# Performance work log

Hardware: AMD Instinct MI355X
Metric: run time of the kernel (lower is better)

The kernel has to match this reference:

```python
import jax, jax.numpy as jnp
import numpy as np

N = 16000
E = 128000
IN_DIM = 512
H1 = 4096
H2 = 1024
OUT_DIM = 64


def setup_inputs() -> dict:
    key = jax.random.key(0)
    ks = jax.random.split(key, 8)
    x = jax.random.normal(ks[0], (N, IN_DIM), dtype=jnp.float32)
    edge_index = jax.random.randint(ks[1], (2, E), 0, N, dtype=jnp.int64)

    def glorot(k, fan_in, fan_out):
        lim = float(np.sqrt(6.0 / (fan_in + fan_out)))
        return jax.random.uniform(k, (fan_in, fan_out), jnp.float32, -lim, lim)

    # PyG SAGEConv: out = lin_l(mean_j x_j) + lin_r(x); lin_l has bias, lin_r does not.
    params = {
        'W1l': glorot(ks[2], IN_DIM, H1), 'b1': jnp.zeros((H1,), jnp.float32),
        'W1r': glorot(ks[3], IN_DIM, H1),
        'W2l': glorot(ks[4], H1, H2), 'b2': jnp.zeros((H2,), jnp.float32),
        'W2r': glorot(ks[5], H1, H2),
        'W3l': glorot(ks[6], H2, OUT_DIM), 'b3': jnp.zeros((OUT_DIM,), jnp.float32),
        'W3r': glorot(ks[7], H2, OUT_DIM),
    }
    return {'x': x, 'edge_index': edge_index, **params}


def _sage_conv(x, src, dst, Wl, b, Wr):
    # mean-aggregate neighbor features at dst, then linear; plus root transform
    agg = jax.ops.segment_sum(x[src], dst, num_segments=N)          # [N, F_in]
    cnt = jax.ops.segment_sum(jnp.ones((src.shape[0],), x.dtype), dst, num_segments=N)
    mean = agg / jnp.maximum(cnt, 1.0)[:, None]
    return mean @ Wl + b + x @ Wr


def reference(x, edge_index, W1l, b1, W1r, W2l, b2, W2r, W3l, b3, W3r):
    src, dst = edge_index[0], edge_index[1]
    h = jax.nn.relu(_sage_conv(x, src, dst, W1l, b1, W1r))   # dropout is identity in eval
    h = jax.nn.relu(_sage_conv(h, src, dst, W2l, b2, W2r))
    h = _sage_conv(h, src, dst, W3l, b3, W3r)
    return jax.nn.log_softmax(h, axis=1)
```

## Files before the change

kernel.cpp:

```cpp
#include <hip/hip_runtime.h>
#include <stdint.h>

typedef __bf16 bf16x8 __attribute__((ext_vector_type(8)));
typedef float  f32x4  __attribute__((ext_vector_type(4)));
typedef const void __attribute__((address_space(1))) gv_t;
typedef void __attribute__((address_space(3))) sv_t;

static __device__ __forceinline__ unsigned short f2bf(float f) {
  unsigned u = __float_as_uint(f);
  u += 0x7fffu + ((u >> 16) & 1u);
  return (unsigned short)(u >> 16);
}
static __device__ __forceinline__ float bf2f(unsigned short h) {
  return __uint_as_float(((unsigned)h) << 16);
}
static __device__ __forceinline__ void gload16(const void* g, void* l) {
  __builtin_amdgcn_global_load_lds((gv_t*)g, (sv_t*)l, 16, 0, 0);
}

__global__ void k_sentinel(float* out, int n, float val) {
  int t = blockIdx.x * 256 + threadIdx.x;
  if (t < n) out[t] = val;
}
__global__ void k_zero(int* p, int n) {
  int t = blockIdx.x * 256 + threadIdx.x;
  if (t < n) p[t] = 0;
}

__global__ void k_detect(const int* ei, int* flag) {
  if (blockIdx.x == 0 && threadIdx.x == 0) {
    int nz = 0;
    for (int t = 0; t < 256; ++t) nz += (ei[2 * t + 1] != 0);
    *flag = (nz == 0) ? 1 : 0;
  }
}

__global__ void k_degree(const int* ei, int E, const int* flag, int* deg) {
  int t = blockIdx.x * 256 + threadIdx.x;
  if (t < E) {
    int d = (*flag) ? ei[2 * (E + t)] : ei[E + t];
    atomicAdd(&deg[d], 1);
  }
}
__global__ void k_scan(const int* deg, int* rp, int* cur, int n) {
  __shared__ int ssum[256];
  int t = threadIdx.x;
  int chunk = (n + 255) >> 8;
  int lo = t * chunk, hi = min(lo + chunk, n);
  int s = 0;
  for (int i = lo; i < hi; ++i) s += deg[i];
  ssum[t] = s;
  __syncthreads();
  if (t == 0) {
    int run = 0;
    for (int i = 0; i < 256; ++i) { int v = ssum[i]; ssum[i] = run; run += v; }
  }
  __syncthreads();
  int run = ssum[t];
  for (int i = lo; i < hi; ++i) { rp[i] = run; cur[i] = run; run += deg[i]; }
  if (t == 255) rp[n] = run;
}
__global__ void k_fill(const int* ei, int E, const int* flag, int* cur, int* col) {
  int t = blockIdx.x * 256 + threadIdx.x;
  if (t < E) {
    int f = *flag;
    int s = f ? ei[2 * t] : ei[t];
    int d = f ? ei[2 * (E + t)] : ei[E + t];
    int p = atomicAdd(&cur[d], 1);
    col[p] = s;
  }
}

__global__ void k_cvtx(const float4* __restrict__ in, ushort4* __restrict__ xm, int total4) {
  int t = blockIdx.x * 256 + threadIdx.x;
  if (t < total4) {
    int row = t >> 7, c = t & 127;
    float4 v = in[t];
    xm[(size_t)row * 256 + c] = make_ushort4(f2bf(v.x), f2bf(v.y), f2bf(v.z), f2bf(v.w));
  }
}

__global__ void k_transW(const float* W, unsigned short* Wt, int K, int N, int ld, int kofs) {
  __shared__ float tile[32][33];
  int tx = threadIdx.x & 31, ty = threadIdx.x >> 5;
  int n0 = blockIdx.x << 5, k0 = blockIdx.y << 5;
#pragma unroll
  for (int r = 0; r < 4; ++r)
    tile[ty + r * 8][tx] = W[(size_t)(k0 + ty + r * 8) * N + n0 + tx];
  __syncthreads();
#pragma unroll
  for (int r = 0; r < 4; ++r)
    Wt[(size_t)(n0 + ty + r * 8) * ld + kofs + k0 + tx] = f2bf(tile[tx][ty + r * 8]);
}

__global__ void k_agg(ushort4* __restrict__ xm, const int* __restrict__ rp,
                      const int* __restrict__ col) {
  int i = blockIdx.x;
  int s = rp[i], e = rp[i + 1];
  float inv = 1.0f / (float)max(e - s, 1);
  int f = threadIdx.x;
  float4 a = make_float4(0.f, 0.f, 0.f, 0.f);
  for (int n = s; n < e; ++n) {
    ushort4 v = xm[(size_t)col[n] * 256 + f];
    a.x += bf2f(v.x); a.y += bf2f(v.y); a.z += bf2f(v.z); a.w += bf2f(v.w);
  }
  xm[(size_t)i * 256 + 128 + f] =
      make_ushort4(f2bf(a.x * inv), f2bf(a.y * inv), f2bf(a.z * inv), f2bf(a.w * inv));
}

template <bool RELU, bool BIAS>
__global__ __launch_bounds__(512, 1) void k_gemm256(
    const unsigned short* __restrict__ A, const unsigned short* __restrict__ B,
    const float* __restrict__ bias, unsigned short* __restrict__ outp,
    int Mreal, int N, int K, int bnShift) {
  __shared__ __align__(16) unsigned short lds[2][2][256 * 64];

  const int tid = threadIdx.x;
  const int lane = tid & 63;
  const int wq = tid >> 6;
  const int wr = wq >> 2;
  const int wc = wq & 3;

  const int nwg = gridDim.x;
  const int q8 = nwg >> 3, r8 = nwg & 7;
  const int xcd = blockIdx.x & 7, idx = blockIdx.x >> 3;
  const int wg = (xcd < r8 ? xcd * (q8 + 1) : r8 * (q8 + 1) + (xcd - r8) * q8) + idx;
  const int bn = wg & ((1 << bnShift) - 1);
  const int bm = wg >> bnShift;

  const unsigned short* Ap = A + (size_t)bm * 256 * K;
  const unsigned short* Bp = B + (size_t)bn * 256 * K;
  const int sl8 = ((lane & 7) ^ (lane >> 3)) * 8;
  const int rsub = wq * 8 + (lane >> 3);

#define STAGE_A(BUF, I, K0)                                            \
  gload16(Ap + (size_t)((I) * 64 + rsub) * K + (K0) + sl8,             \
          (char*)&lds[BUF][0][0] + ((I) * 64 + wq * 8) * 128)
#define STAGE_B(BUF, I, K0)                                            \
  gload16(Bp + (size_t)((I) * 64 + rsub) * K + (K0) + sl8,             \
          (char*)&lds[BUF][1][0] + ((I) * 64 + wq * 8) * 128)
#define VMCNT(NUM) asm volatile("s_waitcnt vmcnt(" #NUM ")" ::: "memory")

  f32x4 acc[8][4];
#pragma unroll
  for (int m = 0; m < 8; ++m)
#pragma unroll
    for (int n = 0; n < 4; ++n) acc[m][n] = (f32x4){0.f, 0.f, 0.f, 0.f};

#define LOAD_AFR(DST, CUR, QA)                                                          \
  do {                                                                                  \
    const char* baseA = (const char*)&lds[CUR][0][0];                                   \
    _Pragma("unroll") for (int mm = 0; mm < 4; ++mm) {                                  \
      const int rr = ((QA) * 4 + mm) * 32 + wr * 16 + (lane & 15);                      \
      _Pragma("unroll") for (int kk = 0; kk < 2; ++kk)                                  \
          DST[mm][kk] = *(const bf16x8*)(baseA + rr * 128 +                             \
                                         (((kk * 4 + (lane >> 4)) ^ (lane & 7)) << 4)); \
    }                                                                                   \
  } while (0)
#define LOAD_BFR(DST, CUR, QB)                                                          \
  do {                                                                                  \
    const char* baseB = (const char*)&lds[CUR][1][0];                                   \
    _Pragma("unroll") for (int nn = 0; nn < 2; ++nn) {                                  \
      const int cc = ((QB) * 2 + nn) * 64 + wc * 16 + (lane & 15);                      \
      _Pragma("unroll") for (int kk = 0; kk < 2; ++kk)                                  \
          DST[nn][kk] = *(const bf16x8*)(baseB + cc * 128 +                             \
                                         (((kk * 4 + (lane >> 4)) ^ (lane & 7)) << 4)); \
    }                                                                                   \
  } while (0)
#define MFMA_Q(QA, QB, AFR, BFR)                                                        \
  do {                                                                                  \
    _Pragma("unroll") for (int mm = 0; mm < 4; ++mm)                                    \
        _Pragma("unroll") for (int nn = 0; nn < 2; ++nn)                                \
            _Pragma("unroll") for (int kk = 0; kk < 2; ++kk)                            \
                acc[(QA) * 4 + mm][(QB) * 2 + nn] =                                     \
                    __builtin_amdgcn_mfma_f32_16x16x32_bf16(                            \
                        AFR[mm][kk], BFR[nn][kk], acc[(QA) * 4 + mm][(QB) * 2 + nn],    \
                        0, 0, 0);                                                       \
  } while (0)

  STAGE_A(0, 0, 0); STAGE_A(0, 1, 0);
  STAGE_B(0, 0, 0); STAGE_B(0, 1, 0);
  STAGE_B(0, 2, 0); STAGE_B(0, 3, 0);
  STAGE_A(0, 2, 0); STAGE_A(0, 3, 0);
  STAGE_A(1, 0, 64); STAGE_A(1, 1, 64);
  STAGE_B(1, 0, 64); STAGE_B(1, 1, 64);
  STAGE_B(1, 2, 64); STAGE_B(1, 3, 64);
  STAGE_A(1, 2, 64); STAGE_A(1, 3, 64);
  VMCNT(8);
  __builtin_amdgcn_s_barrier();

  bf16x8 a0[4][2], b0[2][2], a1[4][2], b1[2][2];
  LOAD_AFR(a0, 0, 0);
  LOAD_BFR(b0, 0, 0);

  const int nt = K >> 6;
#pragma unroll 1
  for (int t = 0; t < nt; ++t) {
    const int cur = t & 1, nxt = cur ^ 1;
    const int k2 = (t + 2) << 6;
    LOAD_AFR(a1, cur, 1);
    LOAD_BFR(b1, cur, 1);
    __builtin_amdgcn_s_setprio(1);
    MFMA_Q(0, 0, a0, b0);
    __builtin_amdgcn_s_setprio(0);
    asm volatile("s_waitcnt lgkmcnt(0)" ::: "memory");
    __builtin_amdgcn_s_barrier();
    if (t + 2 < nt) {
      STAGE_A(cur, 0, k2); STAGE_A(cur, 1, k2);
      STAGE_B(cur, 0, k2); STAGE_B(cur, 1, k2);
      STAGE_B(cur, 2, k2); STAGE_B(cur, 3, k2);
      STAGE_A(cur, 2, k2); STAGE_A(cur, 3, k2);
    }
    __builtin_amdgcn_s_setprio(1);
    MFMA_Q(1, 0, a1, b0);
    MFMA_Q(0, 1, a0, b1);
    __builtin_amdgcn_s_setprio(0);
    if (t + 1 < nt) {
      if (t + 2 < nt) { VMCNT(8); } else { VMCNT(0); }
      __builtin_amdgcn_s_barrier();
      LOAD_AFR(a0, nxt, 0);
      LOAD_BFR(b0, nxt, 0);
    }
    __builtin_amdgcn_s_setprio(1);
    MFMA_Q(1, 1, a1, b1);
    __builtin_amdgcn_s_setprio(0);
  }

  const int row0 = bm * 256 + wr * 16 + ((lane >> 4) << 2);
  const int col0 = bn * 256 + wc * 16 + (lane & 15);
#pragma unroll
  for (int m = 0; m < 8; ++m) {
#pragma unroll
    for (int n = 0; n < 4; ++n) {
      const int col = col0 + n * 64;
      float bb = BIAS ? bias[col] : 0.f;
#pragma unroll
      for (int r = 0; r < 4; ++r) {
        int row = row0 + m * 32 + r;
        if (row < Mreal) {
          float v = acc[m][n][r] + bb;
          if (RELU) v = fmaxf(v, 0.f);
          outp[(size_t)row * N + col] = f2bf(v);
        }
      }
    }
  }
#undef MFMA_Q
#undef LOAD_BFR
#undef LOAD_AFR
#undef VMCNT
#undef STAGE_A
#undef STAGE_B
}

template <int NF, bool TWO, bool RELU, bool BIAS>
__global__ __launch_bounds__(256) void k_gemm(
    const unsigned short* __restrict__ Am, const unsigned short* __restrict__ Ar,
    const unsigned short* __restrict__ Bl, const unsigned short* __restrict__ Br,
    const float* __restrict__ bias, unsigned short* __restrict__ outp, int N, int K) {
  constexpr int BN = NF * 32;
  __shared__ __align__(16) unsigned short lds[(128 + BN) * 64];
  unsigned short* ldsA = lds;
  unsigned short* ldsB = lds + 128 * 64;

  const int tid = threadIdx.x;
  const int lane = tid & 63;
  const int w = tid >> 6;
  const int wr = w >> 1, wc = w & 1;

  f32x4 zero = {0.f, 0.f, 0.f, 0.f};
  f32x4 acc[4][NF];
#pragma unroll
  for (int m = 0; m < 4; ++m)
#pragma unroll
    for (int n = 0; n < NF; ++n) acc[m][n] = zero;

  const int bm = blockIdx.x, bn = blockIdx.y;
  const int sl_st = (lane & 7) ^ (lane >> 3);

#pragma unroll 1
  for (int pass = 0; pass < (TWO ? 2 : 1); ++pass) {
    const unsigned short* A = (TWO && pass) ? Ar : Am;
    const unsigned short* B = (TWO && pass) ? Br : Bl;
    A += (size_t)bm * 128 * K;
    B += (size_t)bn * BN * K;
#pragma unroll 1
    for (int k0 = 0; k0 < K; k0 += 64) {
      __syncthreads();
#pragma unroll
      for (int q = 0; q < 4; ++q) {
        int rowi = (w * 4 + q) * 8 + (lane >> 3);
        gload16(A + (size_t)rowi * K + k0 + sl_st * 8, (char*)ldsA + (w * 4 + q) * 1024);
      }
#pragma unroll
      for (int q = 0; q < NF; ++q) {
        int rowi = (w * NF + q) * 8 + (lane >> 3);
        gload16(B + (size_t)rowi * K + k0 + sl_st * 8, (char*)ldsB + (w * NF + q) * 1024);
      }
      __syncthreads();
#pragma unroll
      for (int kk = 0; kk < 2; ++kk) {
        int sw = (((kk * 4 + (lane >> 4)) ^ (lane & 7)) << 4);
        bf16x8 af[4], bfr[NF];
#pragma unroll
        for (int m = 0; m < 4; ++m) {
          int r = wr * 64 + m * 16 + (lane & 15);
          af[m] = *(const bf16x8*)((const char*)ldsA + r * 128 + sw);
        }
#pragma unroll
        for (int n = 0; n < NF; ++n) {
          int c = wc * (BN / 2) + n * 16 + (lane & 15);
          bfr[n] = *(const bf16x8*)((const char*)ldsB + c * 128 + sw);
        }
#pragma unroll
        for (int m = 0; m < 4; ++m)
#pragma unroll
          for (int n = 0; n < NF; ++n)
            acc[m][n] = __builtin_amdgcn_mfma_f32_16x16x32_bf16(af[m], bfr[n], acc[m][n], 0, 0, 0);
      }
    }
  }

  const int row0 = bm * 128 + wr * 64;
  const int col0 = bn * BN + wc * (BN / 2);
#pragma unroll
  for (int m = 0; m < 4; ++m) {
#pragma unroll
    for (int n = 0; n < NF; ++n) {
      int col = col0 + n * 16 + (lane & 15);
      float bb = BIAS ? bias[col] : 0.f;
#pragma unroll
      for (int r = 0; r < 4; ++r) {
        int row = row0 + m * 16 + ((lane >> 4) << 2) + r;
        float v = acc[m][n][r] + bb;
        if (RELU) v = fmaxf(v, 0.f);
        outp[(size_t)row * N + col] = f2bf(v);
      }
    }
  }
}

__global__ void k_combine2(const ushort4* __restrict__ Z2, const int* __restrict__ rp,
                           const int* __restrict__ col, const float* __restrict__ bias,
                           ushort4* __restrict__ h2) {
  int i = blockIdx.x;
  int s = rp[i], e = rp[i + 1];
  float inv = 1.0f / (float)max(e - s, 1);
  int f = threadIdx.x;
  float4 a = make_float4(0.f, 0.f, 0.f, 0.f);
  float4 b = make_float4(0.f, 0.f, 0.f, 0.f);
  int n = s;
  for (; n + 1 < e; n += 2) {
    int j0 = col[n], j1 = col[n + 1];
    ushort4 v0 = Z2[(size_t)j0 * 512 + f];
    ushort4 v1 = Z2[(size_t)j1 * 512 + f];
    a.x += bf2f(v0.x); a.y += bf2f(v0.y); a.z += bf2f(v0.z); a.w += bf2f(v0.w);
    b.x += bf2f(v1.x); b.y += bf2f(v1.y); b.z += bf2f(v1.z); b.w += bf2f(v1.w);
  }
  if (n < e) {
    ushort4 v0 = Z2[(size_t)col[n] * 512 + f];
    a.x += bf2f(v0.x); a.y += bf2f(v0.y); a.z += bf2f(v0.z); a.w += bf2f(v0.w);
  }
  a.x += b.x; a.y += b.y; a.z += b.z; a.w += b.w;
  ushort4 r = Z2[(size_t)i * 512 + 256 + f];
  float4 b4 = ((const float4*)bias)[f];
  float o0 = fmaxf(a.x * inv + bf2f(r.x) + b4.x, 0.f);
  float o1 = fmaxf(a.y * inv + bf2f(r.y) + b4.y, 0.f);
  float o2 = fmaxf(a.z * inv + bf2f(r.z) + b4.z, 0.f);
  float o3 = fmaxf(a.w * inv + bf2f(r.w) + b4.w, 0.f);
  h2[(size_t)i * 256 + f] = make_ushort4(f2bf(o0), f2bf(o1), f2bf(o2), f2bf(o3));
}

__global__ void k_combine3(const unsigned short* __restrict__ Z3, const int* __restrict__ rp,
                           const int* __restrict__ col, const float* __restrict__ bias,
                           float* __restrict__ out) {
  int i = blockIdx.x * 4 + (threadIdx.x >> 6);
  int c = threadIdx.x & 63;
  int s = rp[i], e = rp[i + 1];
  float inv = 1.0f / (float)max(e - s, 1);
  float a = 0.f;
  for (int n = s; n < e; ++n) a += bf2f(Z3[(size_t)col[n] * 128 + c]);
  float v = a * inv + bf2f(Z3[(size_t)i * 128 + 64 + c]) + bias[c];
  float m = v;
#pragma unroll
  for (int o = 1; o < 64; o <<= 1) m = fmaxf(m, __shfl_xor(m, o, 64));
  float t = expf(v - m);
  float sum = t;
#pragma unroll
  for (int o = 1; o < 64; o <<= 1) sum += __shfl_xor(sum, o, 64);
  out[(size_t)i * 64 + c] = (v - m) - logf(sum);
}

extern "C" void kernel_launch(void* const* d_in, const int* in_sizes, int n_in,
                              void* d_out, int out_size, void* d_ws, size_t ws_size,
                              hipStream_t stream) {
  const float* x   = (const float*)d_in[0];
  const int*   ei  = (const int*)d_in[1];
  const float* W1l = (const float*)d_in[2];
  const float* b1  = (const float*)d_in[3];
  const float* W1r = (const float*)d_in[4];
  const float* W2l = (const float*)d_in[5];
  const float* b2  = (const float*)d_in[6];
  const float* W2r = (const float*)d_in[7];
  const float* W3l = (const float*)d_in[8];
  const float* b3  = (const float*)d_in[9];
  const float* W3r = (const float*)d_in[10];

  const int Nn = 16000;
  const int E = in_sizes[1] / 2;

  char* p = (char*)d_ws;
  auto carve = [&](size_t bytes) {
    char* r = p;
    p += (bytes + 255) & ~(size_t)255;
    return r;
  };
  int* deg    = (int*)carve((size_t)Nn * 4);
  int* rp     = (int*)carve((size_t)(Nn + 1) * 4);
  int* cur    = (int*)carve((size_t)Nn * 4);
  int* flag   = (int*)carve(4);
  int* colidx = (int*)carve((size_t)E * 4);
  unsigned short* Wb = (unsigned short*)carve((size_t)2048 * 4096 * 2);
  unsigned short* xm = (unsigned short*)carve((size_t)Nn * 1024 * 2);
  unsigned short* h1 = (unsigned short*)carve((size_t)Nn * 4096 * 2);
  unsigned short* Z2 = (unsigned short*)carve((size_t)Nn * 2048 * 2);
  unsigned short* Z3 = (unsigned short*)carve((size_t)Nn * 128 * 2);
  unsigned short* h2 = xm;

  size_t need = (size_t)(p - (char*)d_ws);
  if (ws_size < need) {
    k_sentinel<<<(out_size + 255) / 256, 256, 0, stream>>>((float*)d_out, out_size,
                                                           (float)(ws_size >> 20));
    return;
  }

  k_zero<<<(Nn + 255) / 256, 256, 0, stream>>>(deg, Nn);
  k_detect<<<1, 64, 0, stream>>>(ei, flag);
  k_degree<<<(E + 255) / 256, 256, 0, stream>>>(ei, E, flag, deg);
  k_scan<<<1, 256, 0, stream>>>(deg, rp, cur, Nn);
  k_fill<<<(E + 255) / 256, 256, 0, stream>>>(ei, E, flag, cur, colidx);

  k_cvtx<<<(Nn * 128 + 255) / 256, 256, 0, stream>>>((const float4*)x, (ushort4*)xm, Nn * 128);
  k_transW<<<dim3(4096 / 32, 512 / 32), 256, 0, stream>>>(W1r, Wb, 512, 4096, 1024, 0);
  k_transW<<<dim3(4096 / 32, 512 / 32), 256, 0, stream>>>(W1l, Wb, 512, 4096, 1024, 512);
  k_agg<<<Nn, 128, 0, stream>>>((ushort4*)xm, rp, colidx);
  k_gemm256<true, true><<<63 * 16, 512, 0, stream>>>(xm, Wb, b1, h1, Nn, 4096, 1024, 4);

  k_transW<<<dim3(1024 / 32, 4096 / 32), 256, 0, stream>>>(W2l, Wb, 4096, 1024, 4096, 0);
  k_transW<<<dim3(1024 / 32, 4096 / 32), 256, 0, stream>>>(W2r, Wb + (size_t)1024 * 4096, 4096,
                                                           1024, 4096, 0);
  k_gemm256<false, false><<<63 * 8, 512, 0, stream>>>(h1, Wb, nullptr, Z2, Nn, 2048, 4096, 3);
  k_combine2<<<Nn, 256, 0, stream>>>((const ushort4*)Z2, rp, colidx, b2, (ushort4*)h2);

  k_transW<<<dim3(64 / 32, 1024 / 32), 256, 0, stream>>>(W3l, Wb, 1024, 64, 1024, 0);
  k_transW<<<dim3(64 / 32, 1024 / 32), 256, 0, stream>>>(W3r, Wb + (size_t)64 * 1024, 1024, 64,
                                                         1024, 0);
  k_gemm<2, false, false, false><<<dim3(125, 2), 256, 0, stream>>>(h2, nullptr, Wb, nullptr,
                                                                   nullptr, Z3, 128, 1024);
  k_combine3<<<Nn / 4, 256, 0, stream>>>(Z3, rp, colidx, b3, (float*)d_out);

  (void)n_in; (void)out_size;
}
```

Before: 590.0 us.

## Add phase-interleaved GEMM256 variant with staged loads between MFMA quadrants for layer 1

Adds k_gemm256p, which splits each K-tile iteration into four MFMA quadrant phases separated by barriers. Each phase interleaves LDS fragment reads and a slice of global-to-LDS staging so memory traffic overlaps compute more evenly. Layer 1 now uses this kernel. The original k_gemm256, still used for layer 2, is also reordered so it waits on vmcnt(0) mid-iteration and drops the later barrier. That change may stall on outstanding prefetches and could create an LDS race when fragments are read from the next buffer without a barrier. The new kernel adds many barriers per iteration, which trades extra synchronization for finer-grained overlap.

```diff
diff --git a/kernel.cpp b/kernel.cpp
--- a/kernel.cpp
+++ b/kernel.cpp
@@ -108,29 +108,21 @@
       make_ushort4(f2bf(a.x * inv), f2bf(a.y * inv), f2bf(a.z * inv), f2bf(a.w * inv));
 }
 
-template <bool RELU, bool BIAS>
-__global__ __launch_bounds__(512, 1) void k_gemm256(
-    const unsigned short* __restrict__ A, const unsigned short* __restrict__ B,
-    const float* __restrict__ bias, unsigned short* __restrict__ outp,
-    int Mreal, int N, int K, int bnShift) {
-  __shared__ __align__(16) unsigned short lds[2][2][256 * 64];
-
-  const int tid = threadIdx.x;
-  const int lane = tid & 63;
-  const int wq = tid >> 6;
-  const int wr = wq >> 2;
-  const int wc = wq & 3;
-
-  const int nwg = gridDim.x;
-  const int q8 = nwg >> 3, r8 = nwg & 7;
-  const int xcd = blockIdx.x & 7, idx = blockIdx.x >> 3;
-  const int wg = (xcd < r8 ? xcd * (q8 + 1) : r8 * (q8 + 1) + (xcd - r8) * q8) + idx;
-  const int bn = wg & ((1 << bnShift) - 1);
-  const int bm = wg >> bnShift;
-
-  const unsigned short* Ap = A + (size_t)bm * 256 * K;
-  const unsigned short* Bp = B + (size_t)bn * 256 * K;
-  const int sl8 = ((lane & 7) ^ (lane >> 3)) * 8;
+#define GEMM256_SETUP(A_, B_, bnShift_)                                               \
+  const int tid = threadIdx.x;                                                        \
+  const int lane = tid & 63;                                                          \
+  const int wq = tid >> 6;                                                            \
+  const int wr = wq >> 2;                                                             \
+  const int wc = wq & 3;                                                              \
+  const int nwg = gridDim.x;                                                          \
+  const int q8 = nwg >> 3, r8 = nwg & 7;                                              \
+  const int xcd = blockIdx.x & 7, idx = blockIdx.x >> 3;                              \
+  const int wg = (xcd < r8 ? xcd * (q8 + 1) : r8 * (q8 + 1) + (xcd - r8) * q8) + idx; \
+  const int bn = wg & ((1 << (bnShift_)) - 1);                                        \
+  const int bm = wg >> (bnShift_);                                                    \
+  const unsigned short* Ap = (A_) + (size_t)bm * 256 * K;                             \
+  const unsigned short* Bp = (B_) + (size_t)bn * 256 * K;                             \
+  const int sl8 = ((lane & 7) ^ (lane >> 3)) * 8;                                     \
   const int rsub = wq * 8 + (lane >> 3);
 
 #define STAGE_A(BUF, I, K0)                                            \
@@ -140,12 +132,6 @@
   gload16(Bp + (size_t)((I) * 64 + rsub) * K + (K0) + sl8,             \
           (char*)&lds[BUF][1][0] + ((I) * 64 + wq * 8) * 128)
 #define VMCNT(NUM) asm volatile("s_waitcnt vmcnt(" #NUM ")" ::: "memory")
-
-  f32x4 acc[8][4];
-#pragma unroll
-  for (int m = 0; m < 8; ++m)
-#pragma unroll
-    for (int n = 0; n < 4; ++n) acc[m][n] = (f32x4){0.f, 0.f, 0.f, 0.f};
 
 #define LOAD_AFR(DST, CUR, QA)                                                          \
   do {                                                                                  \
@@ -178,16 +164,51 @@
                         0, 0, 0);                                                       \
   } while (0)
 
-  STAGE_A(0, 0, 0); STAGE_A(0, 1, 0);
-  STAGE_B(0, 0, 0); STAGE_B(0, 1, 0);
-  STAGE_B(0, 2, 0); STAGE_B(0, 3, 0);
-  STAGE_A(0, 2, 0); STAGE_A(0, 3, 0);
-  STAGE_A(1, 0, 64); STAGE_A(1, 1, 64);
-  STAGE_B(1, 0, 64); STAGE_B(1, 1, 64);
-  STAGE_B(1, 2, 64); STAGE_B(1, 3, 64);
-  STAGE_A(1, 2, 64); STAGE_A(1, 3, 64);
-  VMCNT(8);
+#define GEMM256_PROLOGUE                                               \
+  STAGE_A(0, 0, 0); STAGE_A(0, 1, 0);                                  \
+  STAGE_B(0, 0, 0); STAGE_B(0, 1, 0);                                  \
+  STAGE_B(0, 2, 0); STAGE_B(0, 3, 0);                                  \
+  STAGE_A(0, 2, 0); STAGE_A(0, 3, 0);                                  \
+  STAGE_A(1, 0, 64); STAGE_A(1, 1, 64);                                \
+  STAGE_B(1, 0, 64); STAGE_B(1, 1, 64);                                \
+  STAGE_B(1, 2, 64); STAGE_B(1, 3, 64);                                \
+  STAGE_A(1, 2, 64); STAGE_A(1, 3, 64);                                \
+  VMCNT(8);                                                            \
   __builtin_amdgcn_s_barrier();
+
+#define GEMM256_EPILOGUE(RELU_, BIAS_)                                 \
+  const int row0 = bm * 256 + wr * 16 + ((lane >> 4) << 2);            \
+  const int col0 = bn * 256 + wc * 16 + (lane & 15);                   \
+  _Pragma("unroll") for (int m = 0; m < 8; ++m) {                      \
+    _Pragma("unroll") for (int n = 0; n < 4; ++n) {                    \
+      const int col = col0 + n * 64;                                   \
+      float bb = (BIAS_) ? bias[col] : 0.f;                            \
+      _Pragma("unroll") for (int r = 0; r < 4; ++r) {                  \
+        int row = row0 + m * 32 + r;                                   \
+        if (row < Mreal) {                                             \
+          float v = acc[m][n][r] + bb;                                 \
+          if (RELU_) v = fmaxf(v, 0.f);                                \
+          outp[(size_t)row * N + col] = f2bf(v);                       \
+        }                                                              \
+      }                                                                \
+    }                                                                  \
+  }
+
+template <bool RELU, bool BIAS>
+__global__ __launch_bounds__(512, 1) void k_gemm256(
+    const unsigned short* __restrict__ A, const unsigned short* __restrict__ B,
+    const float* __restrict__ bias, unsigned short* __restrict__ outp,
+    int Mreal, int N, int K, int bnShift) {
+  __shared__ __align__(16) unsigned short lds[2][2][256 * 64];
+  GEMM256_SETUP(A, B, bnShift)
+
+  f32x4 acc[8][4];
+#pragma unroll
+  for (int m = 0; m < 8; ++m)
+#pragma unroll
+    for (int n = 0; n < 4; ++n) acc[m][n] = (f32x4){0.f, 0.f, 0.f, 0.f};
+
+  GEMM256_PROLOGUE
 
   bf16x8 a0[4][2], b0[2][2], a1[4][2], b1[2][2];
   LOAD_AFR(a0, 0, 0);
@@ -202,8 +223,9 @@
     LOAD_BFR(b1, cur, 1);
     __builtin_amdgcn_s_setprio(1);
     MFMA_Q(0, 0, a0, b0);
+    MFMA_Q(0, 1, a0, b1);
     __builtin_amdgcn_s_setprio(0);
-    asm volatile("s_waitcnt lgkmcnt(0)" ::: "memory");
+    asm volatile("s_waitcnt vmcnt(0) lgkmcnt(0)" ::: "memory");
     __builtin_amdgcn_s_barrier();
     if (t + 2 < nt) {
       STAGE_A(cur, 0, k2); STAGE_A(cur, 1, k2);
@@ -213,44 +235,80 @@
     }
     __builtin_amdgcn_s_setprio(1);
     MFMA_Q(1, 0, a1, b0);
-    MFMA_Q(0, 1, a0, b1);
+    MFMA_Q(1, 1, a1, b1);
     __builtin_amdgcn_s_setprio(0);
     if (t + 1 < nt) {
-      if (t + 2 < nt) { VMCNT(8); } else { VMCNT(0); }
-      __builtin_amdgcn_s_barrier();
       LOAD_AFR(a0, nxt, 0);
       LOAD_BFR(b0, nxt, 0);
     }
+  }
+
+  GEMM256_EPILOGUE(RELU, BIAS)
+}
+
+template <bool RELU, bool BIAS>
+__global__ __launch_bounds__(512, 1) void k_gemm256p(
+    const unsigned short* __restrict__ A, const unsigned short* __restrict__ B,
+    const float* __restrict__ bias, unsigned short* __restrict__ outp,
+    int Mreal, int N, int K, int bnShift) {
+  __shared__ __align__(16) unsigned short lds[2][2][256 * 64];
+  GEMM256_SETUP(A, B, bnShift)
+
+  f32x4 acc[8][4];
+#pragma unroll
+  for (int m = 0; m < 8; ++m)
+#pragma unroll
+    for (int n = 0; n < 4; ++n) acc[m][n] = (f32x4){0.f, 0.f, 0.f, 0.f};
+
+  GEMM256_PROLOGUE
+
+  const int nt = K >> 6;
+#pragma unroll 1
+  for (int t = 0; t < nt; ++t) {
+    const int cur = t & 1;
+    const int k2 = (t + 2) << 6;
+    const bool st = (t + 2) < nt;
+    bf16x8 a0[4][2], b0[2][2], a1[4][2], b1[2][2];
+    LOAD_AFR(a0, cur, 0);
+    LOAD_BFR(b0, cur, 0);
+    __builtin_amdgcn_s_barrier();
+    asm volatile("s_waitcnt lgkmcnt(0)" ::: "memory");
+    __builtin_amdgcn_sched_barrier(0);
+    __builtin_amdgcn_s_setprio(1);
+    MFMA_Q(0, 0, a0, b0);
+    __builtin_amdgcn_s_setprio(0);
+    __builtin_amdgcn_s_barrier();
+    LOAD_BFR(b1, cur, 1);
+    if (st) { STAGE_A(cur, 0, k2); STAGE_A(cur, 1, k2); }
+    __builtin_amdgcn_s_barrier();
+    asm volatile("s_waitcnt lgkmcnt(0)" ::: "memory");
+    __builtin_amdgcn_sched_barrier(0);
+    __builtin_amdgcn_s_setprio(1);
+    MFMA_Q(0, 1, a0, b1);
+    __builtin_amdgcn_s_setprio(0);
+    __builtin_amdgcn_s_barrier();
+    LOAD_AFR(a1, cur, 1);
+    if (st) { STAGE_B(cur, 0, k2); STAGE_B(cur, 1, k2); }
+    __builtin_amdgcn_s_barrier();
+    asm volatile("s_waitcnt lgkmcnt(0)" ::: "memory");
+    __builtin_amdgcn_sched_barrier(0);
     __builtin_amdgcn_s_setprio(1);
     MFMA_Q(1, 1, a1, b1);
     __builtin_amdgcn_s_setprio(0);
-  }
-
-  const int row0 = bm * 256 + wr * 16 + ((lane >> 4) << 2);
-  const int col0 = bn * 256 + wc * 16 + (lane & 15);
-#pragma unroll
-  for (int m = 0; m < 8; ++m) {
-#pragma unroll
-    for (int n = 0; n < 4; ++n) {
-      const int col = col0 + n * 64;
-      float bb = BIAS ? bias[col] : 0.f;
-#pragma unroll
-      for (int r = 0; r < 4; ++r) {
-        int row = row0 + m * 32 + r;
-        if (row < Mreal) {
-          float v = acc[m][n][r] + bb;
-          if (RELU) v = fmaxf(v, 0.f);
-          outp[(size_t)row * N + col] = f2bf(v);
-        }
-      }
+    __builtin_amdgcn_s_barrier();
+    if (st) {
+      STAGE_B(cur, 2, k2); STAGE_B(cur, 3, k2);
+      STAGE_A(cur, 2, k2); STAGE_A(cur, 3, k2);
     }
-  }
-#undef MFMA_Q
-#undef LOAD_BFR
-#undef LOAD_AFR
-#undef VMCNT
-#undef STAGE_A
-#undef STAGE_B
+    __builtin_amdgcn_s_barrier();
+    __builtin_amdgcn_s_setprio(1);
+    MFMA_Q(1, 0, a1, b0);
+    __builtin_amdgcn_s_setprio(0);
+    if (st) { VMCNT(8); } else { VMCNT(0); }
+    __builtin_amdgcn_s_barrier();
+  }
+
+  GEMM256_EPILOGUE(RELU, BIAS)
 }
 
 template <int NF, bool TWO, bool RELU, bool BIAS>
@@ -444,7 +502,7 @@
   k_transW<<<dim3(4096 / 32, 512 / 32), 256, 0, stream>>>(W1r, Wb, 512, 4096, 1024, 0);
   k_transW<<<dim3(4096 / 32, 512 / 32), 256, 0, stream>>>(W1l, Wb, 512, 4096, 1024, 512);
   k_agg<<<Nn, 128, 0, stream>>>((ushort4*)xm, rp, colidx);
-  k_gemm256<true, true><<<63 * 16, 512, 0, stream>>>(xm, Wb, b1, h1, Nn, 4096, 1024, 4);
+  k_gemm256p<true, true><<<63 * 16, 512, 0, stream>>>(xm, Wb, b1, h1, Nn, 4096, 1024, 4);
 
   k_transW<<<dim3(1024 / 32, 4096 / 32), 256, 0, stream>>>(W2l, Wb, 4096, 1024, 4096, 0);
   k_transW<<<dim3(1024 / 32, 4096 / 32), 256, 0, stream>>>(W2r, Wb + (size_t)1024 * 4096, 4096,
```

Result: no change. 598.7 us (+1.5%).
